# Kernel tuning notes

Hardware: AMD Instinct MI355X
Metric: run time of the kernel (lower is better)

The kernel has to match this reference:

```python
import jax, jax.numpy as jnp
import numpy as np

EPS_D = 1e-8   # clamp_min on knn distances
EPS_BN = 1e-5  # BatchNorm eps
K = 3


def _cdist(a, b):
    # a: (B,M,3), b: (B,N,3) -> (B,M,N) euclidean distances
    a2 = jnp.sum(a * a, axis=-1)[:, :, None]
    b2 = jnp.sum(b * b, axis=-1)[:, None, :]
    ab = jnp.einsum('bmd,bnd->bmn', a, b)
    return jnp.sqrt(jnp.maximum(a2 + b2 - 2.0 * ab, 0.0))


def _bn_relu(x, gamma, beta):
    # x: (B,C,N); BatchNorm1d training-mode math (biased batch stats) + ReLU
    mean = jnp.mean(x, axis=(0, 2), keepdims=True)
    var = jnp.mean((x - mean) ** 2, axis=(0, 2), keepdims=True)
    xn = (x - mean) * jax.lax.rsqrt(var + EPS_BN)
    return jax.nn.relu(xn * gamma[None, :, None] + beta[None, :, None])


def setup_inputs() -> dict:
    key = jax.random.key(0)
    ks = jax.random.split(key, 6)
    B, N1, N2, C1, C2 = 8, 8192, 2048, 128, 256
    xyz1 = jax.random.normal(ks[0], (B, N1, 3), dtype=jnp.float32)
    xyz2 = jax.random.normal(ks[1], (B, N2, 3), dtype=jnp.float32)
    feats1 = jax.random.normal(ks[2], (B, C1, N1), dtype=jnp.float32)
    feats2 = jax.random.normal(ks[3], (B, C2, N2), dtype=jnp.float32)
    in_ch = C2 + C1  # 384
    W1 = jax.random.normal(ks[4], (256, in_ch), dtype=jnp.float32) * 0.05
    b1 = jnp.zeros((256,), jnp.float32)
    g1 = jnp.ones((256,), jnp.float32)
    be1 = jnp.zeros((256,), jnp.float32)
    W2 = jax.random.normal(ks[5], (128, 256), dtype=jnp.float32) * 0.05
    b2 = jnp.zeros((128,), jnp.float32)
    g2 = jnp.ones((128,), jnp.float32)
    be2 = jnp.zeros((128,), jnp.float32)
    return {"xyz1": xyz1, "xyz2": xyz2, "feats1": feats1, "feats2": feats2,
            "W1": W1, "b1": b1, "g1": g1, "be1": be1,
            "W2": W2, "b2": b2, "g2": g2, "be2": be2}


def reference(xyz1, xyz2, feats1, feats2, W1, b1, g1, be1, W2, b2, g2, be2):
    # --- KNN interpolation ---
    d = _cdist(xyz1, xyz2)                       # (B,N1,N2)
    _, idx = jax.lax.top_k(-d, K)                # smallest-K indices (B,N1,K)
    knn_d = jnp.take_along_axis(d, idx, axis=2)  # (B,N1,K)
    w = 1.0 / jnp.maximum(knn_d, EPS_D)
    w = w / jnp.sum(w, axis=-1, keepdims=True)
    f2p = jnp.swapaxes(feats2, 1, 2)             # (B,N2,C2)
    neigh = jax.vmap(lambda f, i: f[i])(f2p, idx)  # (B,N1,K,C2)
    out = jnp.einsum('bmk,bmkc->bmc', w, neigh)  # (B,N1,C2)
    out = jnp.swapaxes(out, 1, 2)                # (B,C2,N1)
    out = jnp.concatenate([out, feats1], axis=1) # (B,C2+C1,N1)
    # --- Conv1d(1)-BN-ReLU MLP ---
    h = jnp.einsum('oc,bcn->bon', W1, out) + b1[None, :, None]
    h = _bn_relu(h, g1, be1)
    h = jnp.einsum('oc,bcn->bon', W2, h) + b2[None, :, None]
    h = _bn_relu(h, g2, be2)
    return h
```

## Files before the change

### kernel.cpp

```cpp
#include <hip/hip_runtime.h>

typedef __attribute__((ext_vector_type(8))) short short8;
typedef __attribute__((ext_vector_type(4))) float f32x4;

#define GLDS(gp, lp) __builtin_amdgcn_global_load_lds( \
    (const __attribute__((address_space(1))) void*)(gp), \
    (__attribute__((address_space(3))) void*)(lp), 16, 0, 0)

__device__ __forceinline__ unsigned short f2bf(float f){
    unsigned u = __float_as_uint(f);
    unsigned r = (u + 0x7fffu + ((u >> 16) & 1u)) >> 16;
    return (unsigned short)r;
}
__device__ __forceinline__ float bf2f(unsigned short s){
    return __uint_as_float(((unsigned)s) << 16);
}

__global__ __launch_bounds__(256) void init_kernel(const float* __restrict__ W1, const float* __restrict__ W2,
                                                   unsigned short* __restrict__ W1c, unsigned short* __restrict__ W2c,
                                                   float* __restrict__ stats){
    int i = blockIdx.x * 256 + threadIdx.x;
    if (i < 98304) W1c[i] = f2bf(W1[i]);
    if (i < 32768) W2c[i] = f2bf(W2[i]);
    if (i < 768) stats[i] = 0.f;
}

__global__ __launch_bounds__(256) void knn_kernel(const float* __restrict__ xyz1, const float* __restrict__ xyz2,
                                                  int* __restrict__ oi, float* __restrict__ ow){
    __shared__ float sx[2048], sy[2048], sz[2048];
    __shared__ float sd[64][25];
    __shared__ int   si[64][25];
    int blk = blockIdx.x;
    int b  = blk >> 7;
    int n0 = (blk & 127) << 6;
    const float* p2 = xyz2 + (size_t)b * 2048 * 3;
    for (int j = threadIdx.x; j < 2048; j += 256){
        sx[j] = p2[j*3+0]; sy[j] = p2[j*3+1]; sz[j] = p2[j*3+2];
    }
    __syncthreads();
    int pp = threadIdx.x & 31, sub = threadIdx.x >> 5;
    int pA = n0 + pp;
    const float* qa = xyz1 + ((size_t)b * 8192 + pA) * 3;
    float ax = qa[0], ay = qa[1], az = qa[2];
    float bx = qa[96], by = qa[97], bz = qa[98];
    float A0 = 1e30f, A1 = 1e30f, A2 = 1e30f; int Ai0 = 0, Ai1 = 0, Ai2 = 0;
    float B0 = 1e30f, B1 = 1e30f, B2 = 1e30f; int Bi0 = 0, Bi1 = 0, Bi2 = 0;
    int jb = sub << 8;
#pragma unroll 2
    for (int i = 0; i < 256; i += 4){
        f32x4 cx = *(const f32x4*)&sx[jb + i];
        f32x4 cy = *(const f32x4*)&sy[jb + i];
        f32x4 cz = *(const f32x4*)&sz[jb + i];
#pragma unroll
        for (int u = 0; u < 4; ++u){
            int j = jb + i + u;
            float dxA = ax - cx[u], dyA = ay - cy[u], dzA = az - cz[u];
            float dA = fmaf(dxA, dxA, fmaf(dyA, dyA, dzA * dzA));
            float dxB = bx - cx[u], dyB = by - cy[u], dzB = bz - cz[u];
            float dB = fmaf(dxB, dxB, fmaf(dyB, dyB, dzB * dzB));
            if (dA < A2){
                if (dA < A1){
                    A2 = A1; Ai2 = Ai1;
                    if (dA < A0){ A1 = A0; Ai1 = Ai0; A0 = dA; Ai0 = j; }
                    else        { A1 = dA; Ai1 = j; }
                } else { A2 = dA; Ai2 = j; }
            }
            if (dB < B2){
                if (dB < B1){
                    B2 = B1; Bi2 = Bi1;
                    if (dB < B0){ B1 = B0; Bi1 = Bi0; B0 = dB; Bi0 = j; }
                    else        { B1 = dB; Bi1 = j; }
                } else { B2 = dB; Bi2 = j; }
            }
        }
    }
    int c = sub * 3;
    sd[pp][c] = A0; sd[pp][c+1] = A1; sd[pp][c+2] = A2;
    si[pp][c] = Ai0; si[pp][c+1] = Ai1; si[pp][c+2] = Ai2;
    sd[pp+32][c] = B0; sd[pp+32][c+1] = B1; sd[pp+32][c+2] = B2;
    si[pp+32][c] = Bi0; si[pp+32][c+1] = Bi1; si[pp+32][c+2] = Bi2;
    __syncthreads();
    if (threadIdx.x < 64){
        int lp = threadIdx.x;
        float d0 = 1e30f, d1 = 1e30f, d2 = 1e30f;
        int i0 = 0, i1 = 0, i2 = 0;
#pragma unroll
        for (int k = 0; k < 24; ++k){
            float d = sd[lp][k]; int j = si[lp][k];
            if (d < d2){
                if (d < d1){
                    d2 = d1; i2 = i1;
                    if (d < d0){ d1 = d0; i1 = i0; d0 = d; i0 = j; }
                    else        { d1 = d;  i1 = j; }
                } else { d2 = d; i2 = j; }
            }
        }
        float w0 = 1.f / fmaxf(sqrtf(d0), 1e-8f);
        float w1 = 1.f / fmaxf(sqrtf(d1), 1e-8f);
        float w2 = 1.f / fmaxf(sqrtf(d2), 1e-8f);
        float inv = 1.f / (w0 + w1 + w2);
        int n = n0 + lp;
        size_t pbase = ((size_t)b * 8192 + n) * 3;
        ow[pbase + 0] = w0 * inv; ow[pbase + 1] = w1 * inv; ow[pbase + 2] = w2 * inv;
        oi[pbase + 0] = i0;       oi[pbase + 1] = i1;       oi[pbase + 2] = i2;
    }
}

__global__ __launch_bounds__(256) void transpose_f2_kernel(const float* __restrict__ f2, unsigned short* __restrict__ f2t){
    __shared__ float tile[32][33];
    int b = blockIdx.z, c0 = blockIdx.y * 32, n0 = blockIdx.x * 32;
    int tx = threadIdx.x, ty = threadIdx.y;
    for (int i = 0; i < 32; i += 8)
        tile[ty + i][tx] = f2[((size_t)b * 256 + c0 + ty + i) * 2048 + n0 + tx];
    __syncthreads();
    for (int i = 0; i < 32; i += 8)
        f2t[((size_t)b * 2048 + n0 + ty + i) * 256 + c0 + tx] = f2bf(tile[tx][ty + i]);
}

__global__ __launch_bounds__(256) void transpose_f1_kernel(const float* __restrict__ f1, unsigned short* __restrict__ f1t){
    __shared__ float tile[32][33];
    int b = blockIdx.z, c0 = blockIdx.y * 32, n0 = blockIdx.x * 32;
    int tx = threadIdx.x, ty = threadIdx.y;
    for (int i = 0; i < 32; i += 8)
        tile[ty + i][tx] = f1[((size_t)b * 128 + c0 + ty + i) * 8192 + n0 + tx];
    __syncthreads();
    for (int i = 0; i < 32; i += 8)
        f1t[((size_t)b * 8192 + n0 + ty + i) * 128 + c0 + tx] = f2bf(tile[tx][ty + i]);
}

__global__ __launch_bounds__(256, 2) void gemm1_fused(const unsigned short* __restrict__ f2t,
                                                      const unsigned short* __restrict__ f1t,
                                                      const int* __restrict__ ki, const float* __restrict__ kw,
                                                      const unsigned short* __restrict__ W1c,
                                                      const float* __restrict__ bias,
                                                      unsigned short* __restrict__ h1,
                                                      float* __restrict__ gsum, float* __restrict__ gsq){
    __shared__ unsigned short As[128 * 40];
    __shared__ unsigned short Bs[256 * 32];
    __shared__ int   sIdx[384];
    __shared__ float sW[384];
    __shared__ float sLs[256], sLq[256];
    int tid = threadIdx.x;
    int m0 = blockIdx.x << 7;
    int b  = blockIdx.x >> 6;
    for (int i = tid; i < 384; i += 256){ sIdx[i] = ki[(size_t)m0 * 3 + i]; sW[i] = kw[(size_t)m0 * 3 + i]; }
    sLs[tid] = 0.f; sLq[tid] = 0.f;
    __syncthreads();

    int pt = tid >> 1, hh = tid & 1;
    int i0 = sIdx[pt*3], i1 = sIdx[pt*3+1], i2 = sIdx[pt*3+2];
    float w0 = sW[pt*3], w1 = sW[pt*3+1], w2 = sW[pt*3+2];
    const unsigned short* r0 = f2t + (((size_t)b * 2048 + i0) << 8);
    const unsigned short* r1 = f2t + (((size_t)b * 2048 + i1) << 8);
    const unsigned short* r2 = f2t + (((size_t)b * 2048 + i2) << 8);
    const unsigned short* f1row = f1t + ((size_t)(m0 + pt) << 7);
    unsigned short* awp = As + pt * 40 + hh * 16;

    int srow = tid >> 2, schunk = tid & 3;
    const char* Bb = (const char*)W1c + ((size_t)srow * 384 + schunk * 8) * 2;
    char* Bsl = (char*)Bs + tid * 16;

    int lane = tid & 63, wid = tid >> 6;
    int m_w = (wid >> 1) * 64, n_w = (wid & 1) * 128;
    int lr = lane & 15, lq = lane >> 4;
    f32x4 acc[4][8] = {};

    for (int kt = 0; kt < 12; ++kt){
        size_t ko = (size_t)kt * 64;
        GLDS(Bb + ko,                 Bsl);
        GLDS(Bb + ko + (size_t)49152, Bsl + 4096);
        GLDS(Bb + ko + (size_t)98304, Bsl + 8192);
        GLDS(Bb + ko + (size_t)147456, Bsl + 12288);
        if (kt < 8){
            int cb = kt * 32 + hh * 16;
            uint4 a0 = *(const uint4*)(r0 + cb);
            uint4 a1 = *(const uint4*)(r0 + cb + 8);
            uint4 c0 = *(const uint4*)(r1 + cb);
            uint4 c1 = *(const uint4*)(r1 + cb + 8);
            uint4 d0 = *(const uint4*)(r2 + cb);
            uint4 d1 = *(const uint4*)(r2 + cb + 8);
            uint4 o0, o1;
            const unsigned* ap = (const unsigned*)&a0; const unsigned* cp = (const unsigned*)&c0;
            const unsigned* dp = (const unsigned*)&d0; unsigned* op = (unsigned*)&o0;
#pragma unroll
            for (int u = 0; u < 4; ++u){
                float lo = w0 * bf2f((unsigned short)(ap[u] & 0xffff))
                         + w1 * bf2f((unsigned short)(cp[u] & 0xffff))
                         + w2 * bf2f((unsigned short)(dp[u] & 0xffff));
                float hi = w0 * bf2f((unsigned short)(ap[u] >> 16))
                         + w1 * bf2f((unsigned short)(cp[u] >> 16))
                         + w2 * bf2f((unsigned short)(dp[u] >> 16));
                op[u] = (unsigned)f2bf(lo) | ((unsigned)f2bf(hi) << 16);
            }
            ap = (const unsigned*)&a1; cp = (const unsigned*)&c1;
            dp = (const unsigned*)&d1; op = (unsigned*)&o1;
#pragma unroll
            for (int u = 0; u < 4; ++u){
                float lo = w0 * bf2f((unsigned short)(ap[u] & 0xffff))
                         + w1 * bf2f((unsigned short)(cp[u] & 0xffff))
                         + w2 * bf2f((unsigned short)(dp[u] & 0xffff));
                float hi = w0 * bf2f((unsigned short)(ap[u] >> 16))
                         + w1 * bf2f((unsigned short)(cp[u] >> 16))
                         + w2 * bf2f((unsigned short)(dp[u] >> 16));
                op[u] = (unsigned)f2bf(lo) | ((unsigned)f2bf(hi) << 16);
            }
            *(uint4*)awp = o0;
            *(uint4*)(awp + 8) = o1;
        } else {
            int cb = (kt - 8) * 32 + hh * 16;
            uint4 v0 = *(const uint4*)(f1row + cb);
            uint4 v1 = *(const uint4*)(f1row + cb + 8);
            *(uint4*)awp = v0;
            *(uint4*)(awp + 8) = v1;
        }
        __syncthreads();
        short8 af[4], bfr[8];
#pragma unroll
        for (int mf = 0; mf < 4; ++mf)
            af[mf] = *(const short8*)(As + (m_w + mf * 16 + lr) * 40 + lq * 8);
#pragma unroll
        for (int nf = 0; nf < 8; ++nf)
            bfr[nf] = *(const short8*)(Bs + (n_w + nf * 16 + lr) * 32 + lq * 8);
#pragma unroll
        for (int mf = 0; mf < 4; ++mf)
#pragma unroll
            for (int nf = 0; nf < 8; ++nf)
                acc[mf][nf] = __builtin_amdgcn_mfma_f32_16x16x32_bf16(af[mf], bfr[nf], acc[mf][nf], 0, 0, 0);
        __syncthreads();
    }

#pragma unroll
    for (int nf = 0; nf < 8; ++nf){
        int gc = n_w + nf * 16 + lr;
        float bv = bias[gc];
        float ps = 0.f, pq = 0.f;
#pragma unroll
        for (int mf = 0; mf < 4; ++mf){
            int grow = m0 + m_w + mf * 16 + lq * 4;
#pragma unroll
            for (int r = 0; r < 4; ++r){
                float v = acc[mf][nf][r] + bv;
                h1[(size_t)(grow + r) * 256 + gc] = f2bf(v);
                ps += v; pq += v * v;
            }
        }
        ps += __shfl_xor(ps, 16); ps += __shfl_xor(ps, 32);
        pq += __shfl_xor(pq, 16); pq += __shfl_xor(pq, 32);
        if (lq == 0){ atomicAdd(&sLs[gc], ps); atomicAdd(&sLq[gc], pq); }
    }
    __syncthreads();
    atomicAdd(&gsum[tid], sLs[tid]);
    atomicAdd(&gsq[tid],  sLq[tid]);
}

__global__ void bnprep_kernel(const float* __restrict__ s1, const float* __restrict__ q1,
                              const float* __restrict__ g1, const float* __restrict__ be1,
                              float* __restrict__ sc, float* __restrict__ sh){
    int c = threadIdx.x;
    const float inv = 1.0f / 65536.0f;
    float m = s1[c] * inv;
    float v = q1[c] * inv - m * m;
    float rs = rsqrtf(v + 1e-5f);
    float s = g1[c] * rs;
    sc[c] = s; sh[c] = be1[c] - m * s;
}

__global__ __launch_bounds__(256, 2) void gemm2_fused(const unsigned short* __restrict__ h1,
                                                      const unsigned short* __restrict__ W2c,
                                                      const float* __restrict__ bias,
                                                      const float* __restrict__ sc1, const float* __restrict__ sh1,
                                                      float* __restrict__ h2,
                                                      float* __restrict__ gsum, float* __restrict__ gsq){
    __shared__ unsigned short As[128 * 40];
    __shared__ unsigned short Bs[128 * 32];
    __shared__ float ssc[256], ssh[256];
    __shared__ float sLs[128], sLq[128];
    int tid = threadIdx.x;
    int m0 = blockIdx.x << 7;
    ssc[tid] = sc1[tid]; ssh[tid] = sh1[tid];
    if (tid < 128){ sLs[tid] = 0.f; sLq[tid] = 0.f; }
    __syncthreads();

    int pt = tid >> 1, hh = tid & 1;
    const unsigned short* hrow = h1 + ((size_t)(m0 + pt) << 8);
    unsigned short* awp = As + pt * 40 + hh * 16;

    int srow = tid >> 2, schunk = tid & 3;
    const char* Bb = (const char*)W2c + ((size_t)srow * 256 + schunk * 8) * 2;
    char* Bsl = (char*)Bs + tid * 16;

    int lane = tid & 63, wid = tid >> 6;
    int m_w = (wid >> 1) * 64, n_w = (wid & 1) * 64;
    int lr = lane & 15, lq = lane >> 4;
    f32x4 acc[4][4] = {};

    for (int kt = 0; kt < 8; ++kt){
        size_t ko = (size_t)kt * 64;
        GLDS(Bb + ko,                Bsl);
        GLDS(Bb + ko + (size_t)32768, Bsl + 4096);
        int cb = kt * 32 + hh * 16;
        uint4 v0 = *(const uint4*)(hrow + cb);
        uint4 v1 = *(const uint4*)(hrow + cb + 8);
        uint4 o0, o1;
        const unsigned* vp = (const unsigned*)&v0; unsigned* op = (unsigned*)&o0;
#pragma unroll
        for (int u = 0; u < 4; ++u){
            int cc = cb + 2 * u;
            float lo = fmaxf(bf2f((unsigned short)(vp[u] & 0xffff)) * ssc[cc]     + ssh[cc],     0.f);
            float hi = fmaxf(bf2f((unsigned short)(vp[u] >> 16))    * ssc[cc + 1] + ssh[cc + 1], 0.f);
            op[u] = (unsigned)f2bf(lo) | ((unsigned)f2bf(hi) << 16);
        }
        vp = (const unsigned*)&v1; op = (unsigned*)&o1;
#pragma unroll
        for (int u = 0; u < 4; ++u){
            int cc = cb + 8 + 2 * u;
            float lo = fmaxf(bf2f((unsigned short)(vp[u] & 0xffff)) * ssc[cc]     + ssh[cc],     0.f);
            float hi = fmaxf(bf2f((unsigned short)(vp[u] >> 16))    * ssc[cc + 1] + ssh[cc + 1], 0.f);
            op[u] = (unsigned)f2bf(lo) | ((unsigned)f2bf(hi) << 16);
        }
        *(uint4*)awp = o0;
        *(uint4*)(awp + 8) = o1;
        __syncthreads();
        short8 af[4], bfr[4];
#pragma unroll
        for (int mf = 0; mf < 4; ++mf)
            af[mf] = *(const short8*)(As + (m_w + mf * 16 + lr) * 40 + lq * 8);
#pragma unroll
        for (int nf = 0; nf < 4; ++nf)
            bfr[nf] = *(const short8*)(Bs + (n_w + nf * 16 + lr) * 32 + lq * 8);
#pragma unroll
        for (int mf = 0; mf < 4; ++mf)
#pragma unroll
            for (int nf = 0; nf < 4; ++nf)
                acc[mf][nf] = __builtin_amdgcn_mfma_f32_16x16x32_bf16(af[mf], bfr[nf], acc[mf][nf], 0, 0, 0);
        __syncthreads();
    }

#pragma unroll
    for (int nf = 0; nf < 4; ++nf){
        int gc = n_w + nf * 16 + lr;
        float bv = bias[gc];
        float ps = 0.f, pq = 0.f;
#pragma unroll
        for (int mf = 0; mf < 4; ++mf){
            int grow = m0 + m_w + mf * 16 + lq * 4;
#pragma unroll
            for (int r = 0; r < 4; ++r){
                float v = acc[mf][nf][r] + bv;
                h2[(size_t)(grow + r) * 128 + gc] = v;
                ps += v; pq += v * v;
            }
        }
        ps += __shfl_xor(ps, 16); ps += __shfl_xor(ps, 32);
        pq += __shfl_xor(pq, 16); pq += __shfl_xor(pq, 32);
        if (lq == 0){ atomicAdd(&sLs[gc], ps); atomicAdd(&sLq[gc], pq); }
    }
    __syncthreads();
    if (tid < 128){
        atomicAdd(&gsum[tid], sLs[tid]);
        atomicAdd(&gsq[tid],  sLq[tid]);
    }
}

__global__ __launch_bounds__(256) void bn2_transpose_kernel(const float* __restrict__ h2, const float* __restrict__ gsum,
                                                            const float* __restrict__ gsq, const float* __restrict__ g2,
                                                            const float* __restrict__ be2, float* __restrict__ out){
    __shared__ float tile[32][33];
    const float inv = 1.0f / 65536.0f;
    int b = blockIdx.z, o0 = blockIdx.y * 32, n0 = blockIdx.x * 32;
    int tx = threadIdx.x, ty = threadIdx.y;
    for (int i = 0; i < 32; i += 8)
        tile[ty + i][tx] = h2[((size_t)b * 8192 + n0 + ty + i) * 128 + o0 + tx];
    __syncthreads();
    for (int i = 0; i < 32; i += 8){
        int ch = o0 + ty + i;
        float m = gsum[ch] * inv;
        float va = gsq[ch] * inv - m * m;
        float rs = rsqrtf(va + 1e-5f);
        float sc = g2[ch] * rs, sh = be2[ch] - m * sc;
        float v = fmaxf(tile[tx][ty + i] * sc + sh, 0.f);
        out[((size_t)b * 128 + ch) * 8192 + n0 + tx] = v;
    }
}

extern "C" void kernel_launch(void* const* d_in, const int* in_sizes, int n_in,
                              void* d_out, int out_size, void* d_ws, size_t ws_size,
                              hipStream_t stream){
    const float* xyz1   = (const float*)d_in[0];
    const float* xyz2   = (const float*)d_in[1];
    const float* feats1 = (const float*)d_in[2];
    const float* feats2 = (const float*)d_in[3];
    const float* W1  = (const float*)d_in[4];
    const float* b1  = (const float*)d_in[5];
    const float* g1  = (const float*)d_in[6];
    const float* be1 = (const float*)d_in[7];
    const float* W2  = (const float*)d_in[8];
    const float* b2  = (const float*)d_in[9];
    const float* g2  = (const float*)d_in[10];
    const float* be2 = (const float*)d_in[11];
    float* out = (float*)d_out;

    char* p = (char*)d_ws;
    auto take = [&](size_t bytes) -> char* {
        char* r = p; p += (bytes + 255) & ~(size_t)255; return r;
    };
    unsigned short* W1c = (unsigned short*)take((size_t)98304 * 2);
    unsigned short* W2c = (unsigned short*)take((size_t)32768 * 2);
    int*   ki    = (int*)take((size_t)65536 * 3 * 4);
    float* kw    = (float*)take((size_t)65536 * 3 * 4);
    float* stats = (float*)take(768 * 4);
    float* scsh  = (float*)take(512 * 4);
    unsigned short* f2t = (unsigned short*)take((size_t)8 * 2048 * 256 * 2);
    unsigned short* f1t = (unsigned short*)take((size_t)65536 * 128 * 2);
    unsigned short* h1  = (unsigned short*)take((size_t)65536 * 256 * 2);
    float* h2 = (float*)take((size_t)65536 * 128 * 4);

    float* s1 = stats, *q1 = stats + 256, *s2 = stats + 512, *q2 = stats + 640;
    float* sc1 = scsh, *sh1 = scsh + 256;

    init_kernel<<<dim3(384), 256, 0, stream>>>(W1, W2, W1c, W2c, stats);
    knn_kernel<<<dim3(1024), 256, 0, stream>>>(xyz1, xyz2, ki, kw);
    transpose_f2_kernel<<<dim3(64, 8, 8), dim3(32, 8), 0, stream>>>(feats2, f2t);
    transpose_f1_kernel<<<dim3(256, 4, 8), dim3(32, 8), 0, stream>>>(feats1, f1t);
    gemm1_fused<<<dim3(512), 256, 0, stream>>>(f2t, f1t, ki, kw, W1c, b1, h1, s1, q1);
    bnprep_kernel<<<dim3(1), 256, 0, stream>>>(s1, q1, g1, be1, sc1, sh1);
    gemm2_fused<<<dim3(512), 256, 0, stream>>>(h1, W2c, b2, sc1, sh1, h2, s2, q2);
    bn2_transpose_kernel<<<dim3(256, 4, 8), dim3(32, 8), 0, stream>>>(h2, s2, q2, g2, be2, out);
}
```

Before: 258.7 us.

## Double-buffer GEMM tiles, halve M-tile, and use expanded-norm KNN distance

The two fused GEMM kernels now double-buffer their A and B shared-memory tiles. The next k-slice's gather, interpolation or BN-ReLU and the global-to-LDS weight loads are issued while the current MFMAs run, which removes one barrier per iteration. The M tile drops from 128 to 64 rows, doubling the grid and raising the occupancy hints to help fill the CUs. The KNN inner loop switches to a |c|^2 - 2a·c form that shares the candidate norm across two queries and adds |a|^2 back only for the final weights. That form may change neighbor selection slightly because of rounding.

```diff
diff --git a/kernel.cpp b/kernel.cpp
--- a/kernel.cpp
+++ b/kernel.cpp
@@ -43,6 +43,8 @@
     const float* qa = xyz1 + ((size_t)b * 8192 + pA) * 3;
     float ax = qa[0], ay = qa[1], az = qa[2];
     float bx = qa[96], by = qa[97], bz = qa[98];
+    float nax = -2.f*ax, nay = -2.f*ay, naz = -2.f*az;
+    float nbx = -2.f*bx, nby = -2.f*by, nbz = -2.f*bz;
     float A0 = 1e30f, A1 = 1e30f, A2 = 1e30f; int Ai0 = 0, Ai1 = 0, Ai2 = 0;
     float B0 = 1e30f, B1 = 1e30f, B2 = 1e30f; int Bi0 = 0, Bi1 = 0, Bi2 = 0;
     int jb = sub << 8;
@@ -54,23 +56,22 @@
 #pragma unroll
         for (int u = 0; u < 4; ++u){
             int j = jb + i + u;
-            float dxA = ax - cx[u], dyA = ay - cy[u], dzA = az - cz[u];
-            float dA = fmaf(dxA, dxA, fmaf(dyA, dyA, dzA * dzA));
-            float dxB = bx - cx[u], dyB = by - cy[u], dzB = bz - cz[u];
-            float dB = fmaf(dxB, dxB, fmaf(dyB, dyB, dzB * dzB));
-            if (dA < A2){
-                if (dA < A1){
+            float c2 = fmaf(cx[u], cx[u], fmaf(cy[u], cy[u], cz[u]*cz[u]));
+            float tA = fmaf(nax, cx[u], fmaf(nay, cy[u], fmaf(naz, cz[u], c2)));
+            float tB = fmaf(nbx, cx[u], fmaf(nby, cy[u], fmaf(nbz, cz[u], c2)));
+            if (tA < A2){
+                if (tA < A1){
                     A2 = A1; Ai2 = Ai1;
-                    if (dA < A0){ A1 = A0; Ai1 = Ai0; A0 = dA; Ai0 = j; }
-                    else        { A1 = dA; Ai1 = j; }
-                } else { A2 = dA; Ai2 = j; }
-            }
-            if (dB < B2){
-                if (dB < B1){
+                    if (tA < A0){ A1 = A0; Ai1 = Ai0; A0 = tA; Ai0 = j; }
+                    else        { A1 = tA; Ai1 = j; }
+                } else { A2 = tA; Ai2 = j; }
+            }
+            if (tB < B2){
+                if (tB < B1){
                     B2 = B1; Bi2 = Bi1;
-                    if (dB < B0){ B1 = B0; Bi1 = Bi0; B0 = dB; Bi0 = j; }
-                    else        { B1 = dB; Bi1 = j; }
-                } else { B2 = dB; Bi2 = j; }
+                    if (tB < B0){ B1 = B0; Bi1 = Bi0; B0 = tB; Bi0 = j; }
+                    else        { B1 = tB; Bi1 = j; }
+                } else { B2 = tB; Bi2 = j; }
             }
         }
     }
@@ -95,9 +96,12 @@
                 } else { d2 = d; i2 = j; }
             }
         }
-        float w0 = 1.f / fmaxf(sqrtf(d0), 1e-8f);
-        float w1 = 1.f / fmaxf(sqrtf(d1), 1e-8f);
-        float w2 = 1.f / fmaxf(sqrtf(d2), 1e-8f);
+        const float* q = xyz1 + ((size_t)b * 8192 + n0 + lp) * 3;
+        float q2 = fmaf(q[0], q[0], fmaf(q[1], q[1], q[2]*q[2]));
+        float e0 = fmaxf(q2 + d0, 0.f), e1 = fmaxf(q2 + d1, 0.f), e2 = fmaxf(q2 + d2, 0.f);
+        float w0 = 1.f / fmaxf(sqrtf(e0), 1e-8f);
+        float w1 = 1.f / fmaxf(sqrtf(e1), 1e-8f);
+        float w2 = 1.f / fmaxf(sqrtf(e2), 1e-8f);
         float inv = 1.f / (w0 + w1 + w2);
         int n = n0 + lp;
         size_t pbase = ((size_t)b * 8192 + n) * 3;
@@ -128,126 +132,127 @@
         f1t[((size_t)b * 8192 + n0 + ty + i) * 128 + c0 + tx] = f2bf(tile[tx][ty + i]);
 }
 
-__global__ __launch_bounds__(256, 2) void gemm1_fused(const unsigned short* __restrict__ f2t,
+__global__ __launch_bounds__(256, 3) void gemm1_fused(const unsigned short* __restrict__ f2t,
                                                       const unsigned short* __restrict__ f1t,
                                                       const int* __restrict__ ki, const float* __restrict__ kw,
                                                       const unsigned short* __restrict__ W1c,
                                                       const float* __restrict__ bias,
                                                       unsigned short* __restrict__ h1,
                                                       float* __restrict__ gsum, float* __restrict__ gsq){
-    __shared__ unsigned short As[128 * 40];
-    __shared__ unsigned short Bs[256 * 32];
-    __shared__ int   sIdx[384];
-    __shared__ float sW[384];
+    __shared__ unsigned short As[2][64 * 40];
+    __shared__ unsigned short Bs[2][256 * 32];
+    __shared__ int   sIdx[192];
+    __shared__ float sW[192];
     __shared__ float sLs[256], sLq[256];
     int tid = threadIdx.x;
-    int m0 = blockIdx.x << 7;
-    int b  = blockIdx.x >> 6;
-    for (int i = tid; i < 384; i += 256){ sIdx[i] = ki[(size_t)m0 * 3 + i]; sW[i] = kw[(size_t)m0 * 3 + i]; }
+    int m0 = blockIdx.x << 6;
+    int b  = m0 >> 13;
+    if (tid < 192){ sIdx[tid] = ki[(size_t)m0 * 3 + tid]; sW[tid] = kw[(size_t)m0 * 3 + tid]; }
     sLs[tid] = 0.f; sLq[tid] = 0.f;
     __syncthreads();
 
-    int pt = tid >> 1, hh = tid & 1;
+    int pt = tid >> 2, qq = tid & 3;
     int i0 = sIdx[pt*3], i1 = sIdx[pt*3+1], i2 = sIdx[pt*3+2];
     float w0 = sW[pt*3], w1 = sW[pt*3+1], w2 = sW[pt*3+2];
-    const unsigned short* r0 = f2t + (((size_t)b * 2048 + i0) << 8);
-    const unsigned short* r1 = f2t + (((size_t)b * 2048 + i1) << 8);
-    const unsigned short* r2 = f2t + (((size_t)b * 2048 + i2) << 8);
-    const unsigned short* f1row = f1t + ((size_t)(m0 + pt) << 7);
-    unsigned short* awp = As + pt * 40 + hh * 16;
-
-    int srow = tid >> 2, schunk = tid & 3;
-    const char* Bb = (const char*)W1c + ((size_t)srow * 384 + schunk * 8) * 2;
-    char* Bsl = (char*)Bs + tid * 16;
+    const unsigned short* r0 = f2t + (((size_t)b * 2048 + i0) << 8) + qq * 8;
+    const unsigned short* r1 = f2t + (((size_t)b * 2048 + i1) << 8) + qq * 8;
+    const unsigned short* r2 = f2t + (((size_t)b * 2048 + i2) << 8) + qq * 8;
+    const unsigned short* f1row = f1t + ((size_t)(m0 + pt) << 7) + qq * 8;
+    const char* Bb = (const char*)W1c + (size_t)(tid >> 2) * 768 + (size_t)(tid & 3) * 16;
 
     int lane = tid & 63, wid = tid >> 6;
-    int m_w = (wid >> 1) * 64, n_w = (wid & 1) * 128;
+    int n_w = wid * 64;
     int lr = lane & 15, lq = lane >> 4;
-    f32x4 acc[4][8] = {};
+    f32x4 acc[4][4] = {};
+
+    auto interp3 = [&](uint4 a, uint4 c, uint4 d) -> uint4 {
+        uint4 o;
+        const unsigned* ap = (const unsigned*)&a; const unsigned* cp = (const unsigned*)&c;
+        const unsigned* dp = (const unsigned*)&d; unsigned* op = (unsigned*)&o;
+#pragma unroll
+        for (int u = 0; u < 4; ++u){
+            float lo = w0 * bf2f((unsigned short)(ap[u] & 0xffff))
+                     + w1 * bf2f((unsigned short)(cp[u] & 0xffff))
+                     + w2 * bf2f((unsigned short)(dp[u] & 0xffff));
+            float hi = w0 * bf2f((unsigned short)(ap[u] >> 16))
+                     + w1 * bf2f((unsigned short)(cp[u] >> 16))
+                     + w2 * bf2f((unsigned short)(dp[u] >> 16));
+            op[u] = (unsigned)f2bf(lo) | ((unsigned)f2bf(hi) << 16);
+        }
+        return o;
+    };
+
+    {
+        uint4 a = *(const uint4*)r0, c = *(const uint4*)r1, d = *(const uint4*)r2;
+        *(uint4*)(&As[0][pt * 40 + qq * 8]) = interp3(a, c, d);
+#pragma unroll
+        for (int cc = 0; cc < 4; ++cc)
+            GLDS(Bb + (size_t)cc * 49152, (char*)Bs[0] + cc * 4096 + tid * 16);
+    }
+    __syncthreads();
 
     for (int kt = 0; kt < 12; ++kt){
-        size_t ko = (size_t)kt * 64;
-        GLDS(Bb + ko,                 Bsl);
-        GLDS(Bb + ko + (size_t)49152, Bsl + 4096);
-        GLDS(Bb + ko + (size_t)98304, Bsl + 8192);
-        GLDS(Bb + ko + (size_t)147456, Bsl + 12288);
-        if (kt < 8){
-            int cb = kt * 32 + hh * 16;
-            uint4 a0 = *(const uint4*)(r0 + cb);
-            uint4 a1 = *(const uint4*)(r0 + cb + 8);
-            uint4 c0 = *(const uint4*)(r1 + cb);
-            uint4 c1 = *(const uint4*)(r1 + cb + 8);
-            uint4 d0 = *(const uint4*)(r2 + cb);
-            uint4 d1 = *(const uint4*)(r2 + cb + 8);
-            uint4 o0, o1;
-            const unsigned* ap = (const unsigned*)&a0; const unsigned* cp = (const unsigned*)&c0;
-            const unsigned* dp = (const unsigned*)&d0; unsigned* op = (unsigned*)&o0;
-#pragma unroll
-            for (int u = 0; u < 4; ++u){
-                float lo = w0 * bf2f((unsigned short)(ap[u] & 0xffff))
-                         + w1 * bf2f((unsigned short)(cp[u] & 0xffff))
-                         + w2 * bf2f((unsigned short)(dp[u] & 0xffff));
-                float hi = w0 * bf2f((unsigned short)(ap[u] >> 16))
-                         + w1 * bf2f((unsigned short)(cp[u] >> 16))
-                         + w2 * bf2f((unsigned short)(dp[u] >> 16));
-                op[u] = (unsigned)f2bf(lo) | ((unsigned)f2bf(hi) << 16);
-            }
-            ap = (const unsigned*)&a1; cp = (const unsigned*)&c1;
-            dp = (const unsigned*)&d1; op = (unsigned*)&o1;
-#pragma unroll
-            for (int u = 0; u < 4; ++u){
-                float lo = w0 * bf2f((unsigned short)(ap[u] & 0xffff))
-                         + w1 * bf2f((unsigned short)(cp[u] & 0xffff))
-                         + w2 * bf2f((unsigned short)(dp[u] & 0xffff));
-                float hi = w0 * bf2f((unsigned short)(ap[u] >> 16))
-                         + w1 * bf2f((unsigned short)(cp[u] >> 16))
-                         + w2 * bf2f((unsigned short)(dp[u] >> 16));
-                op[u] = (unsigned)f2bf(lo) | ((unsigned)f2bf(hi) << 16);
-            }
-            *(uint4*)awp = o0;
-            *(uint4*)(awp + 8) = o1;
-        } else {
-            int cb = (kt - 8) * 32 + hh * 16;
-            uint4 v0 = *(const uint4*)(f1row + cb);
-            uint4 v1 = *(const uint4*)(f1row + cb + 8);
-            *(uint4*)awp = v0;
-            *(uint4*)(awp + 8) = v1;
+        int cur = kt & 1;
+        uint4 pa, pc, pd;
+        bool hasNext = kt < 11;
+        int nk = kt + 1;
+        if (hasNext){
+            if (nk < 8){
+                pa = *(const uint4*)(r0 + nk * 32);
+                pc = *(const uint4*)(r1 + nk * 32);
+                pd = *(const uint4*)(r2 + nk * 32);
+            } else {
+                pa = *(const uint4*)(f1row + (nk - 8) * 32);
+            }
+#pragma unroll
+            for (int cc = 0; cc < 4; ++cc)
+                GLDS(Bb + (size_t)cc * 49152 + nk * 64, (char*)Bs[cur ^ 1] + cc * 4096 + tid * 16);
+        }
+        short8 af[4], bfr[4];
+#pragma unroll
+        for (int mf = 0; mf < 4; ++mf)
+            af[mf] = *(const short8*)(&As[cur][(mf * 16 + lr) * 40 + lq * 8]);
+#pragma unroll
+        for (int nf = 0; nf < 4; ++nf)
+            bfr[nf] = *(const short8*)(&Bs[cur][(n_w + nf * 16 + lr) * 32 + lq * 8]);
+#pragma unroll
+        for (int mf = 0; mf < 4; ++mf)
+#pragma unroll
+            for (int nf = 0; nf < 4; ++nf)
+                acc[mf][nf] = __builtin_amdgcn_mfma_f32_16x16x32_bf16(af[mf], bfr[nf], acc[mf][nf], 0, 0, 0);
+        if (hasNext){
+            uint4 o = (nk < 8) ? interp3(pa, pc, pd) : pa;
+            *(uint4*)(&As[cur ^ 1][pt * 40 + qq * 8]) = o;
         }
         __syncthreads();
-        short8 af[4], bfr[8];
-#pragma unroll
-        for (int mf = 0; mf < 4; ++mf)
-            af[mf] = *(const short8*)(As + (m_w + mf * 16 + lr) * 40 + lq * 8);
-#pragma unroll
-        for (int nf = 0; nf < 8; ++nf)
-            bfr[nf] = *(const short8*)(Bs + (n_w + nf * 16 + lr) * 32 + lq * 8);
-#pragma unroll
-        for (int mf = 0; mf < 4; ++mf)
-#pragma unroll
-            for (int nf = 0; nf < 8; ++nf)
-                acc[mf][nf] = __builtin_amdgcn_mfma_f32_16x16x32_bf16(af[mf], bfr[nf], acc[mf][nf], 0, 0, 0);
-        __syncthreads();
-    }
-
-#pragma unroll
-    for (int nf = 0; nf < 8; ++nf){
-        int gc = n_w + nf * 16 + lr;
-        float bv = bias[gc];
+    }
+
+    float bv[4];
+#pragma unroll
+    for (int nf = 0; nf < 4; ++nf) bv[nf] = bias[n_w + nf * 16 + lr];
+#pragma unroll
+    for (int nf = 0; nf < 4; ++nf){
         float ps = 0.f, pq = 0.f;
 #pragma unroll
-        for (int mf = 0; mf < 4; ++mf){
-            int grow = m0 + m_w + mf * 16 + lq * 4;
+        for (int mf = 0; mf < 4; ++mf)
 #pragma unroll
             for (int r = 0; r < 4; ++r){
-                float v = acc[mf][nf][r] + bv;
-                h1[(size_t)(grow + r) * 256 + gc] = f2bf(v);
+                float v = acc[mf][nf][r] + bv[nf];
                 ps += v; pq += v * v;
             }
-        }
         ps += __shfl_xor(ps, 16); ps += __shfl_xor(ps, 32);
         pq += __shfl_xor(pq, 16); pq += __shfl_xor(pq, 32);
-        if (lq == 0){ atomicAdd(&sLs[gc], ps); atomicAdd(&sLq[gc], pq); }
-    }
+        if (lq == 0){ atomicAdd(&sLs[n_w + nf * 16 + lr], ps); atomicAdd(&sLq[n_w + nf * 16 + lr], pq); }
+    }
+#pragma unroll
+    for (int mf = 0; mf < 4; ++mf)
+#pragma unroll
+        for (int r = 0; r < 4; ++r){
+            size_t rb = (size_t)(m0 + mf * 16 + lq * 4 + r) * 256 + n_w + lr;
+#pragma unroll
+            for (int nf = 0; nf < 4; ++nf)
+                h1[rb + nf * 16] = f2bf(acc[mf][nf][r] + bv[nf]);
+        }
     __syncthreads();
     atomicAdd(&gsum[tid], sLs[tid]);
     atomicAdd(&gsq[tid],  sLq[tid]);
@@ -265,44 +270,34 @@
     sc[c] = s; sh[c] = be1[c] - m * s;
 }
 
-__global__ __launch_bounds__(256, 2) void gemm2_fused(const unsigned short* __restrict__ h1,
+__global__ __launch_bounds__(256, 4) void gemm2_fused(const unsigned short* __restrict__ h1,
                                                       const unsigned short* __restrict__ W2c,
                                                       const float* __restrict__ bias,
                                                       const float* __restrict__ sc1, const float* __restrict__ sh1,
                                                       float* __restrict__ h2,
                                                       float* __restrict__ gsum, float* __restrict__ gsq){
-    __shared__ unsigned short As[128 * 40];
-    __shared__ unsigned short Bs[128 * 32];
+    __shared__ unsigned short As[2][64 * 40];
+    __shared__ unsigned short Bs[2][128 * 32];
     __shared__ float ssc[256], ssh[256];
     __shared__ float sLs[128], sLq[128];
     int tid = threadIdx.x;
-    int m0 = blockIdx.x << 7;
+    int m0 = blockIdx.x << 6;
     ssc[tid] = sc1[tid]; ssh[tid] = sh1[tid];
     if (tid < 128){ sLs[tid] = 0.f; sLq[tid] = 0.f; }
     __syncthreads();
 
-    int pt = tid >> 1, hh = tid & 1;
-    const unsigned short* hrow = h1 + ((size_t)(m0 + pt) << 8);
-    unsigned short* awp = As + pt * 40 + hh * 16;
-
-    int srow = tid >> 2, schunk = tid & 3;
-    const char* Bb = (const char*)W2c + ((size_t)srow * 256 + schunk * 8) * 2;
-    char* Bsl = (char*)Bs + tid * 16;
+    int pt = tid >> 2, qq = tid & 3;
+    const unsigned short* hrow = h1 + ((size_t)(m0 + pt) << 8) + qq * 8;
+    const char* Bb = (const char*)W2c + (size_t)(tid >> 2) * 512 + (size_t)(tid & 3) * 16;
 
     int lane = tid & 63, wid = tid >> 6;
-    int m_w = (wid >> 1) * 64, n_w = (wid & 1) * 64;
+    int n_w = wid * 32;
     int lr = lane & 15, lq = lane >> 4;
-    f32x4 acc[4][4] = {};
-
-    for (int kt = 0; kt < 8; ++kt){
-        size_t ko = (size_t)kt * 64;
-        GLDS(Bb + ko,                Bsl);
-        GLDS(Bb + ko + (size_t)32768, Bsl + 4096);
-        int cb = kt * 32 + hh * 16;
-        uint4 v0 = *(const uint4*)(hrow + cb);
-        uint4 v1 = *(const uint4*)(hrow + cb + 8);
-        uint4 o0, o1;
-        const unsigned* vp = (const unsigned*)&v0; unsigned* op = (unsigned*)&o0;
+    f32x4 acc[4][2] = {};
+
+    auto bnrelu = [&](uint4 v, int cb) -> uint4 {
+        uint4 o;
+        const unsigned* vp = (const unsigned*)&v; unsigned* op = (unsigned*)&o;
 #pragma unroll
         for (int u = 0; u < 4; ++u){
             int cc = cb + 2 * u;
@@ -310,51 +305,72 @@
             float hi = fmaxf(bf2f((unsigned short)(vp[u] >> 16))    * ssc[cc + 1] + ssh[cc + 1], 0.f);
             op[u] = (unsigned)f2bf(lo) | ((unsigned)f2bf(hi) << 16);
         }
-        vp = (const unsigned*)&v1; op = (unsigned*)&o1;
-#pragma unroll
-        for (int u = 0; u < 4; ++u){
-            int cc = cb + 8 + 2 * u;
-            float lo = fmaxf(bf2f((unsigned short)(vp[u] & 0xffff)) * ssc[cc]     + ssh[cc],     0.f);
-            float hi = fmaxf(bf2f((unsigned short)(vp[u] >> 16))    * ssc[cc + 1] + ssh[cc + 1], 0.f);
-            op[u] = (unsigned)f2bf(lo) | ((unsigned)f2bf(hi) << 16);
-        }
-        *(uint4*)awp = o0;
-        *(uint4*)(awp + 8) = o1;
+        return o;
+    };
+
+    {
+        uint4 v = *(const uint4*)hrow;
+        *(uint4*)(&As[0][pt * 40 + qq * 8]) = bnrelu(v, qq * 8);
+#pragma unroll
+        for (int cc = 0; cc < 2; ++cc)
+            GLDS(Bb + (size_t)cc * 32768, (char*)Bs[0] + cc * 4096 + tid * 16);
+    }
+    __syncthreads();
+
+    for (int kt = 0; kt < 8; ++kt){
+        int cur = kt & 1;
+        uint4 pv;
+        bool hasNext = kt < 7;
+        int nk = kt + 1;
+        if (hasNext){
+            pv = *(const uint4*)(hrow + nk * 32);
+#pragma unroll
+            for (int cc = 0; cc < 2; ++cc)
+                GLDS(Bb + (size_t)cc * 32768 + nk * 64, (char*)Bs[cur ^ 1] + cc * 4096 + tid * 16);
+        }
+        short8 af[4], bfr[2];
+#pragma unroll
+        for (int mf = 0; mf < 4; ++mf)
+            af[mf] = *(const short8*)(&As[cur][(mf * 16 + lr) * 40 + lq * 8]);
+#pragma unroll
+        for (int nf = 0; nf < 2; ++nf)
+            bfr[nf] = *(const short8*)(&Bs[cur][(n_w + nf * 16 + lr) * 32 + lq * 8]);
+#pragma unroll
+        for (int mf = 0; mf < 4; ++mf)
+#pragma unroll
+            for (int nf = 0; nf < 2; ++nf)
+                acc[mf][nf] = __builtin_amdgcn_mfma_f32_16x16x32_bf16(af[mf], bfr[nf], acc[mf][nf], 0, 0, 0);
+        if (hasNext)
+            *(uint4*)(&As[cur ^ 1][pt * 40 + qq * 8]) = bnrelu(pv, nk * 32 + qq * 8);
         __syncthreads();
-        short8 af[4], bfr[4];
-#pragma unroll
-        for (int mf = 0; mf < 4; ++mf)
-            af[mf] = *(const short8*)(As + (m_w + mf * 16 + lr) * 40 + lq * 8);
-#pragma unroll
-        for (int nf = 0; nf < 4; ++nf)
-            bfr[nf] = *(const short8*)(Bs + (n_w + nf * 16 + lr) * 32 + lq * 8);
-#pragma unroll
-        for (int mf = 0; mf < 4; ++mf)
-#pragma unroll
-            for (int nf = 0; nf < 4; ++nf)
-                acc[mf][nf] = __builtin_amdgcn_mfma_f32_16x16x32_bf16(af[mf], bfr[nf], acc[mf][nf], 0, 0, 0);
-        __syncthreads();
-    }
-
-#pragma unroll
-    for (int nf = 0; nf < 4; ++nf){
-        int gc = n_w + nf * 16 + lr;
-        float bv = bias[gc];
+    }
+
+    float bv[2];
+#pragma unroll
+    for (int nf = 0; nf < 2; ++nf) bv[nf] = bias[n_w + nf * 16 + lr];
+#pragma unroll
+    for (int nf = 0; nf < 2; ++nf){
         float ps = 0.f, pq = 0.f;
 #pragma unroll
-        for (int mf = 0; mf < 4; ++mf){
-            int grow = m0 + m_w + mf * 16 + lq * 4;
+        for (int mf = 0; mf < 4; ++mf)
 #pragma unroll
             for (int r = 0; r < 4; ++r){
-                float v = acc[mf][nf][r] + bv;
-                h2[(size_t)(grow + r) * 128 + gc] = v;
+                float v = acc[mf][nf][r] + bv[nf];
                 ps += v; pq += v * v;
             }
-        }
         ps += __shfl_xor(ps, 16); ps += __shfl_xor(ps, 32);
         pq += __shfl_xor(pq, 16); pq += __shfl_xor(pq, 32);
-        if (lq == 0){ atomicAdd(&sLs[gc], ps); atomicAdd(&sLq[gc], pq); }
-    }
+        if (lq == 0){ atomicAdd(&sLs[n_w + nf * 16 + lr], ps); atomicAdd(&sLq[n_w + nf * 16 + lr], pq); }
+    }
+#pragma unroll
+    for (int mf = 0; mf < 4; ++mf)
+#pragma unroll
+        for (int r = 0; r < 4; ++r){
+            size_t rb = (size_t)(m0 + mf * 16 + lq * 4 + r) * 128 + n_w + lr;
+#pragma unroll
+            for (int nf = 0; nf < 2; ++nf)
+                h2[rb + nf * 16] = acc[mf][nf][r] + bv[nf];
+        }
     __syncthreads();
     if (tid < 128){
         atomicAdd(&gsum[tid], sLs[tid]);
@@ -422,8 +438,8 @@
     knn_kernel<<<dim3(1024), 256, 0, stream>>>(xyz1, xyz2, ki, kw);
     transpose_f2_kernel<<<dim3(64, 8, 8), dim3(32, 8), 0, stream>>>(feats2, f2t);
     transpose_f1_kernel<<<dim3(256, 4, 8), dim3(32, 8), 0, stream>>>(feats1, f1t);
-    gemm1_fused<<<dim3(512), 256, 0, stream>>>(f2t, f1t, ki, kw, W1c, b1, h1, s1, q1);
+    gemm1_fused<<<dim3(1024), 256, 0, stream>>>(f2t, f1t, ki, kw, W1c, b1, h1, s1, q1);
     bnprep_kernel<<<dim3(1), 256, 0, stream>>>(s1, q1, g1, be1, sc1, sh1);
-    gemm2_fused<<<dim3(512), 256, 0, stream>>>(h1, W2c, b2, sc1, sh1, h2, s2, q2);
+    gemm2_fused<<<dim3(1024), 256, 0, stream>>>(h1, W2c, b2, sc1, sh1, h2, s2, q2);
     bn2_transpose_kernel<<<dim3(256, 4, 8), dim3(32, 8), 0, stream>>>(h2, s2, q2, g2, be2, out);
 }
```

Result: slower. 274.2 us (+6.0%).
